# Optimization experiments

Measured on AMD Instinct MI355X. Metric: run time of the kernel, lower is better.

Reference implementation:

```python
import jax, jax.numpy as jnp
import numpy as np

TEMPERATURE = 0.5


def setup_inputs() -> dict:
    key = jax.random.key(0)
    k1, k2 = jax.random.split(key)
    N, D = 8192, 128
    features = jax.random.normal(k1, (N, D), dtype=jnp.float32)
    labels = jax.random.randint(k2, (N,), 0, 10, dtype=jnp.int64)
    return {"features": features, "labels": labels}


def reference(features, labels):
    # cosine similarity via normalized matmul (fused form of the broadcasted version)
    eps = 1e-8
    norm = jnp.maximum(jnp.linalg.norm(features, axis=-1, keepdims=True), eps)
    fn = features / norm
    sim = jnp.einsum('id,jd->ij', fn, fn) / TEMPERATURE  # [N, N]

    pos_mask = labels[:, None] == labels[None, :]        # [N, N] bool
    pos_f = pos_mask.astype(sim.dtype)
    neg_f = 1.0 - pos_f

    exp_pos = jnp.exp(sim * pos_f)                       # [N, N]
    exp_neg = jnp.sum(jnp.exp(sim * neg_f), axis=1, keepdims=True)  # [N, 1]

    loss_mat = -jnp.log(exp_pos / (exp_pos + exp_neg))   # [N, N]
    # mean over positive entries (jit-safe masked mean)
    num_pos = jnp.sum(pos_f)
    loss = jnp.sum(loss_mat * pos_f) / num_pos
    return loss
```

## Files before the change

kernel.cpp:

```cpp
#include <hip/hip_runtime.h>
#include <hip/hip_bf16.h>
#include <math.h>

#define NROWS 8192
#define DIM 128
#define BM 128
#define BN 128
#define CS 8
#define COLS_PER_SLAB (NROWS / CS)
#define CT_ITERS (COLS_PER_SLAB / BN)
#define RS (NROWS / BM)
#define SCALE 1.69864368f
#define LN2F 0.69314718056f

typedef __attribute__((ext_vector_type(8))) short bf16x8;
typedef __attribute__((ext_vector_type(4))) float f32x4;

#define VMCNT0 asm volatile("s_waitcnt vmcnt(0)" ::: "memory")
#define BAR __builtin_amdgcn_s_barrier()

__device__ __forceinline__ void gload16(const void* g, void* l) {
  __builtin_amdgcn_global_load_lds(
      (const __attribute__((address_space(1))) void*)g,
      (__attribute__((address_space(3))) void*)l, 16, 0, 0);
}

__device__ __forceinline__ void stageA(const ushort* __restrict__ fnb, int row0,
                                       char* tile, int t) {
  const char* gb = reinterpret_cast<const char*>(fnb) + (size_t)row0 * 256;
#pragma unroll
  for (int i = 0; i < 8; ++i) {
    int q = t + 256 * i;
    int row = q >> 4, c = q & 15;
    gload16(gb + row * 256 + ((c ^ (row & 7)) << 4), tile + q * 16);
  }
}

__device__ __forceinline__ void stageBh(const ushort* __restrict__ fnb, int j0, int kh,
                                        char* buf, int t) {
  const char* gb = reinterpret_cast<const char*>(fnb) + (size_t)j0 * 256 + kh * 128;
#pragma unroll
  for (int i = 0; i < 4; ++i) {
    int q = t + 256 * i;
    int row = q >> 3, c = q & 7;
    gload16(gb + row * 256 + ((c ^ (row & 7)) << 4), buf + q * 16);
  }
}

__global__ __launch_bounds__(256) void k_norm(const float* __restrict__ f,
                                              __hip_bfloat16* __restrict__ fnb,
                                              float* __restrict__ losssum) {
  if (blockIdx.x == 0 && threadIdx.x == 0) losssum[0] = 0.f;
  int wave = threadIdx.x >> 6;
  int lane = threadIdx.x & 63;
  int row = blockIdx.x * 4 + wave;
  const float* src = f + (size_t)row * DIM;
  float v0 = src[lane];
  float v1 = src[lane + 64];
  float ss = v0 * v0 + v1 * v1;
#pragma unroll
  for (int o = 32; o > 0; o >>= 1) ss += __shfl_down(ss, o);
  ss = __shfl(ss, 0);
  float inv = SCALE / fmaxf(sqrtf(ss), 1e-8f);
  __hip_bfloat16* dst = fnb + (size_t)row * DIM;
  dst[lane] = __float2bfloat16(v0 * inv);
  dst[lane + 64] = __float2bfloat16(v1 * inv);
}

__global__ __launch_bounds__(256, 2) void k_main(
    const ushort* __restrict__ fnb, const int* __restrict__ lab,
    float* __restrict__ P, float* __restrict__ Ps) {
  __shared__ char lds[65536];
  char* Bbuf0 = lds + 32768;
  char* Bbuf1 = lds + 49152;

  const int t = threadIdx.x;
  const int lane = t & 63;
  const int w = t >> 6;
  const int wm = w >> 1, wn = w & 1;
  const int g = lane >> 4, li16 = lane & 15;
  const int cs = blockIdx.x;
  const int i0 = blockIdx.y * BM;
  const int jslab = cs * COLS_PER_SLAB;

  stageA(fnb, i0, lds, t);
  stageBh(fnb, jslab, 0, Bbuf0, t);

  int lr[4][4];
#pragma unroll
  for (int m = 0; m < 4; ++m)
#pragma unroll
    for (int r = 0; r < 4; ++r)
      lr[m][r] = lab[i0 + wm * 64 + m * 16 + g * 4 + r];

  float a_tot[4][4] = {}, a_pos[4][4] = {};
  float s_sim = 0.f;

  VMCNT0;
  BAR;

#define COMPUTE(buf, khA)                                                        \
  _Pragma("unroll") for (int ks = 0; ks < 2; ++ks) {                             \
    const int kc = ((khA)*2 + ks) * 4 + g;                                       \
    bf16x8 af[4], bf[4];                                                         \
    _Pragma("unroll") for (int m = 0; m < 4; ++m) {                              \
      int r = wm * 64 + m * 16 + li16;                                           \
      af[m] = *reinterpret_cast<const bf16x8*>(lds + r * 256 + ((kc ^ (r & 7)) << 4)); \
    }                                                                            \
    _Pragma("unroll") for (int n = 0; n < 4; ++n) {                              \
      int r2 = wn * 64 + n * 16 + li16;                                          \
      bf[n] = *reinterpret_cast<const bf16x8*>((buf) + r2 * 128 + (((ks * 4 + g) ^ (r2 & 7)) << 4)); \
    }                                                                            \
    _Pragma("unroll") for (int m = 0; m < 4; ++m)                                \
      _Pragma("unroll") for (int n = 0; n < 4; ++n)                              \
        acc[m][n] = __builtin_amdgcn_mfma_f32_16x16x32_bf16(af[m], bf[n], acc[m][n], 0, 0, 0); \
  }

#pragma unroll 1
  for (int ct = 0; ct < CT_ITERS; ++ct) {
    const int j0 = jslab + ct * BN;

    f32x4 acc[4][4];
#pragma unroll
    for (int m = 0; m < 4; ++m)
#pragma unroll
      for (int n = 0; n < 4; ++n) acc[m][n] = (f32x4){0.f, 0.f, 0.f, 0.f};

    stageBh(fnb, j0, 1, Bbuf1, t);
    COMPUTE(Bbuf0, 0);
    VMCNT0;
    BAR;

    if (ct + 1 < CT_ITERS) stageBh(fnb, j0 + BN, 0, Bbuf0, t);
    COMPUTE(Bbuf1, 1);

#pragma unroll
    for (int n = 0; n < 4; ++n) {
      const int lc = lab[j0 + wn * 64 + n * 16 + li16];
#pragma unroll
      for (int m = 0; m < 4; ++m)
#pragma unroll
        for (int r = 0; r < 4; ++r) {
          float u = acc[m][n][r];
          float E = __builtin_exp2f(u);
          float msk = (lr[m][r] == lc) ? 1.f : 0.f;
          a_tot[m][r] += E;
          a_pos[m][r] = fmaf(msk, E, a_pos[m][r]);
          s_sim = fmaf(msk, u, s_sim);
        }
    }
    VMCNT0;
    BAR;
  }
#undef COMPUTE

#pragma unroll
  for (int m = 0; m < 4; ++m)
#pragma unroll
    for (int r = 0; r < 4; ++r)
#pragma unroll
      for (int off = 8; off > 0; off >>= 1) {
        a_tot[m][r] += __shfl_xor(a_tot[m][r], off);
        a_pos[m][r] += __shfl_xor(a_pos[m][r], off);
      }
#pragma unroll
  for (int off = 32; off > 0; off >>= 1) s_sim += __shfl_xor(s_sim, off);

  __syncthreads();
  float(*red)[2][2] = reinterpret_cast<float(*)[2][2]>(lds);
  float* sS = reinterpret_cast<float*>(lds + 4096);
  if (li16 == 0) {
#pragma unroll
    for (int m = 0; m < 4; ++m)
#pragma unroll
      for (int r = 0; r < 4; ++r) {
        int rl = wm * 64 + m * 16 + g * 4 + r;
        red[rl][wn][0] = a_tot[m][r];
        red[rl][wn][1] = a_pos[m][r];
      }
  }
  if (lane == 0) sS[w] = s_sim;
  __syncthreads();
  if (wn == 0 && li16 == 0) {
#pragma unroll
    for (int m = 0; m < 4; ++m)
#pragma unroll
      for (int r = 0; r < 4; ++r) {
        int rl = wm * 64 + m * 16 + g * 4 + r;
        float* dst = P + ((size_t)cs * NROWS + (i0 + rl)) * 2;
        dst[0] = red[rl][0][0] + red[rl][1][0];
        dst[1] = red[rl][0][1] + red[rl][1][1];
      }
  }
  if (t == 0) Ps[blockIdx.y * CS + cs] = sS[0] + sS[1] + sS[2] + sS[3];
}

__global__ __launch_bounds__(1024) void k_rowfinal(
    const float* __restrict__ P, const int* __restrict__ lab,
    float* __restrict__ losssum) {
  __shared__ int sh[16][16];
  __shared__ int hist_s[16];
  __shared__ float sred[1024];
  const int t = threadIdx.x;
  const int w = t >> 6;
  if ((t & 63) < 16) sh[w][t & 63] = 0;
  __syncthreads();
#pragma unroll
  for (int it = 0; it < NROWS / 1024; ++it)
    atomicAdd(&sh[w][lab[t + it * 1024]], 1);
  __syncthreads();
  if (t < 16) {
    int s = 0;
#pragma unroll
    for (int x = 0; x < 16; ++x) s += sh[x][t];
    hist_s[t] = s;
  }
  __syncthreads();

  int i = blockIdx.x * 1024 + t;
  float st = 0.f, sp = 0.f;
#pragma unroll
  for (int cs = 0; cs < CS; ++cs) {
    const float* p = P + ((size_t)cs * NROWS + i) * 2;
    st += p[0];
    sp += p[1];
  }
  float cnt = (float)hist_s[lab[i]];
  float negtot = st - sp + cnt;
  float li = cnt * logf(negtot) + sp / negtot;
  sred[t] = li;
  __syncthreads();
  for (int s2 = 512; s2 > 0; s2 >>= 1) {
    if (t < s2) sred[t] += sred[t + s2];
    __syncthreads();
  }
  if (t == 0) {
    atomicAdd(&losssum[0], sred[0]);
    if (blockIdx.x == 0) {
      int np = 0;
#pragma unroll
      for (int c = 0; c < 10; ++c) np += hist_s[c] * hist_s[c];
      losssum[1] = (float)np;
    }
  }
}

__global__ __launch_bounds__(512) void k_out(const float* __restrict__ losssum,
                                             const float* __restrict__ Ps,
                                             float* __restrict__ out) {
  __shared__ float sred[512];
  const int t = threadIdx.x;
  sred[t] = Ps[t];
  __syncthreads();
  for (int s = 256; s > 0; s >>= 1) {
    if (t < s) sred[t] += sred[t + s];
    __syncthreads();
  }
  if (t == 0) out[0] = (losssum[0] - LN2F * sred[0]) / losssum[1];
}

extern "C" void kernel_launch(void* const* d_in, const int* in_sizes, int n_in,
                              void* d_out, int out_size, void* d_ws, size_t ws_size,
                              hipStream_t stream) {
  const float* feat = (const float*)d_in[0];
  const int* lab = (const int*)d_in[1];
  float* out = (float*)d_out;
  char* ws = (char*)d_ws;

  __hip_bfloat16* fnb = (__hip_bfloat16*)ws;
  size_t off = (size_t)NROWS * DIM * 2;
  float* P = (float*)(ws + off); off += (size_t)CS * NROWS * 2 * 4;
  float* Ps = (float*)(ws + off); off += (size_t)CS * RS * 4;
  float* losssum = (float*)(ws + off);

  k_norm<<<NROWS / 4, 256, 0, stream>>>(feat, fnb, losssum);
  k_main<<<dim3(CS, RS), 256, 0, stream>>>((const ushort*)fnb, lab, P, Ps);
  k_rowfinal<<<NROWS / 1024, 1024, 0, stream>>>(P, lab, losssum);
  k_out<<<1, 512, 0, stream>>>(losssum, Ps, out);
}
```

Before: 52.15 us.

## Use 8 waves per block in main GEMM kernel and raise MFMA priority

```diff
diff --git a/kernel.cpp b/kernel.cpp
--- a/kernel.cpp
+++ b/kernel.cpp
@@ -29,8 +29,8 @@
                                        char* tile, int t) {
   const char* gb = reinterpret_cast<const char*>(fnb) + (size_t)row0 * 256;
 #pragma unroll
-  for (int i = 0; i < 8; ++i) {
-    int q = t + 256 * i;
+  for (int i = 0; i < 4; ++i) {
+    int q = t + 512 * i;
     int row = q >> 4, c = q & 15;
     gload16(gb + row * 256 + ((c ^ (row & 7)) << 4), tile + q * 16);
   }
@@ -40,8 +40,8 @@
                                         char* buf, int t) {
   const char* gb = reinterpret_cast<const char*>(fnb) + (size_t)j0 * 256 + kh * 128;
 #pragma unroll
-  for (int i = 0; i < 4; ++i) {
-    int q = t + 256 * i;
+  for (int i = 0; i < 2; ++i) {
+    int q = t + 512 * i;
     int row = q >> 3, c = q & 7;
     gload16(gb + row * 256 + ((c ^ (row & 7)) << 4), buf + q * 16);
   }
@@ -67,24 +67,25 @@
   dst[lane + 64] = __float2bfloat16(v1 * inv);
 }
 
-__global__ __launch_bounds__(256, 2) void k_main(
+__global__ __launch_bounds__(512, 4) void k_main(
     const ushort* __restrict__ fnb, const int* __restrict__ lab,
     float* __restrict__ P, float* __restrict__ Ps) {
   __shared__ char lds[65536];
-  char* Bbuf0 = lds + 32768;
-  char* Bbuf1 = lds + 49152;
+  char* Bb0 = lds + 32768;
+  char* Bb1 = lds + 49152;
 
   const int t = threadIdx.x;
   const int lane = t & 63;
   const int w = t >> 6;
-  const int wm = w >> 1, wn = w & 1;
+  const int wm = w >> 2;
+  const int wn = w & 3;
   const int g = lane >> 4, li16 = lane & 15;
   const int cs = blockIdx.x;
   const int i0 = blockIdx.y * BM;
   const int jslab = cs * COLS_PER_SLAB;
 
   stageA(fnb, i0, lds, t);
-  stageBh(fnb, jslab, 0, Bbuf0, t);
+  stageBh(fnb, jslab, 0, Bb0, t);
 
   int lr[4][4];
 #pragma unroll
@@ -99,20 +100,20 @@
   VMCNT0;
   BAR;
 
-#define COMPUTE(buf, khA)                                                        \
+#define COMPUTE(buf, kh)                                                         \
   _Pragma("unroll") for (int ks = 0; ks < 2; ++ks) {                             \
-    const int kc = ((khA)*2 + ks) * 4 + g;                                       \
-    bf16x8 af[4], bf[4];                                                         \
+    const int kc = (kh) * 8 + ks * 4 + g;                                        \
+    bf16x8 af[4], bf[2];                                                         \
     _Pragma("unroll") for (int m = 0; m < 4; ++m) {                              \
       int r = wm * 64 + m * 16 + li16;                                           \
       af[m] = *reinterpret_cast<const bf16x8*>(lds + r * 256 + ((kc ^ (r & 7)) << 4)); \
     }                                                                            \
-    _Pragma("unroll") for (int n = 0; n < 4; ++n) {                              \
-      int r2 = wn * 64 + n * 16 + li16;                                          \
+    _Pragma("unroll") for (int n = 0; n < 2; ++n) {                              \
+      int r2 = wn * 32 + n * 16 + li16;                                          \
       bf[n] = *reinterpret_cast<const bf16x8*>((buf) + r2 * 128 + (((ks * 4 + g) ^ (r2 & 7)) << 4)); \
     }                                                                            \
     _Pragma("unroll") for (int m = 0; m < 4; ++m)                                \
-      _Pragma("unroll") for (int n = 0; n < 4; ++n)                              \
+      _Pragma("unroll") for (int n = 0; n < 2; ++n)                              \
         acc[m][n] = __builtin_amdgcn_mfma_f32_16x16x32_bf16(af[m], bf[n], acc[m][n], 0, 0, 0); \
   }
 
@@ -120,23 +121,27 @@
   for (int ct = 0; ct < CT_ITERS; ++ct) {
     const int j0 = jslab + ct * BN;
 
-    f32x4 acc[4][4];
+    f32x4 acc[4][2];
 #pragma unroll
     for (int m = 0; m < 4; ++m)
 #pragma unroll
-      for (int n = 0; n < 4; ++n) acc[m][n] = (f32x4){0.f, 0.f, 0.f, 0.f};
-
-    stageBh(fnb, j0, 1, Bbuf1, t);
-    COMPUTE(Bbuf0, 0);
+      for (int n = 0; n < 2; ++n) acc[m][n] = (f32x4){0.f, 0.f, 0.f, 0.f};
+
+    stageBh(fnb, j0, 1, Bb1, t);
+    __builtin_amdgcn_s_setprio(1);
+    COMPUTE(Bb0, 0);
+    __builtin_amdgcn_s_setprio(0);
     VMCNT0;
     BAR;
 
-    if (ct + 1 < CT_ITERS) stageBh(fnb, j0 + BN, 0, Bbuf0, t);
-    COMPUTE(Bbuf1, 1);
-
-#pragma unroll
-    for (int n = 0; n < 4; ++n) {
-      const int lc = lab[j0 + wn * 64 + n * 16 + li16];
+    if (ct + 1 < CT_ITERS) stageBh(fnb, j0 + BN, 0, Bb0, t);
+    __builtin_amdgcn_s_setprio(1);
+    COMPUTE(Bb1, 1);
+    __builtin_amdgcn_s_setprio(0);
+
+#pragma unroll
+    for (int n = 0; n < 2; ++n) {
+      const int lc = lab[j0 + wn * 32 + n * 16 + li16];
 #pragma unroll
       for (int m = 0; m < 4; ++m)
 #pragma unroll
@@ -167,8 +172,8 @@
   for (int off = 32; off > 0; off >>= 1) s_sim += __shfl_xor(s_sim, off);
 
   __syncthreads();
-  float(*red)[2][2] = reinterpret_cast<float(*)[2][2]>(lds);
-  float* sS = reinterpret_cast<float*>(lds + 4096);
+  float(*red)[4][2] = reinterpret_cast<float(*)[4][2]>(lds);
+  float* sS = reinterpret_cast<float*>(lds + 8192);
   if (li16 == 0) {
 #pragma unroll
     for (int m = 0; m < 4; ++m)
@@ -188,11 +193,16 @@
       for (int r = 0; r < 4; ++r) {
         int rl = wm * 64 + m * 16 + g * 4 + r;
         float* dst = P + ((size_t)cs * NROWS + (i0 + rl)) * 2;
-        dst[0] = red[rl][0][0] + red[rl][1][0];
-        dst[1] = red[rl][0][1] + red[rl][1][1];
+        dst[0] = red[rl][0][0] + red[rl][1][0] + red[rl][2][0] + red[rl][3][0];
+        dst[1] = red[rl][0][1] + red[rl][1][1] + red[rl][2][1] + red[rl][3][1];
       }
   }
-  if (t == 0) Ps[blockIdx.y * CS + cs] = sS[0] + sS[1] + sS[2] + sS[3];
+  if (t == 0) {
+    float s = 0.f;
+#pragma unroll
+    for (int x = 0; x < 8; ++x) s += sS[x];
+    Ps[blockIdx.y * CS + cs] = s;
+  }
 }
 
 __global__ __launch_bounds__(1024) void k_rowfinal(
@@ -274,7 +284,7 @@
   float* losssum = (float*)(ws + off);
 
   k_norm<<<NROWS / 4, 256, 0, stream>>>(feat, fnb, losssum);
-  k_main<<<dim3(CS, RS), 256, 0, stream>>>((const ushort*)fnb, lab, P, Ps);
+  k_main<<<dim3(CS, RS), 512, 0, stream>>>((const ushort*)fnb, lab, P, Ps);
   k_rowfinal<<<NROWS / 1024, 1024, 0, stream>>>(P, lab, losssum);
   k_out<<<1, 512, 0, stream>>>(losssum, Ps, out);
 }
```

New measurement: 55.92 us. +7.2%, slower.

## Sort rows by label to skip mask work on label-disjoint tiles

Applied to the files above, without the earlier changes.

```diff
diff --git a/kernel.cpp b/kernel.cpp
--- a/kernel.cpp
+++ b/kernel.cpp
@@ -47,10 +47,69 @@
   }
 }
 
+__global__ __launch_bounds__(1024) void k_perm(const int* __restrict__ lab,
+                                               int* __restrict__ perm,
+                                               int* __restrict__ labs_s,
+                                               float* __restrict__ losssum) {
+  __shared__ int sh[16][16];
+  __shared__ int wcount[16][10];
+  __shared__ int baseRun[10];
+  const int t = threadIdx.x;
+  const int w = t >> 6;
+  const int lane = t & 63;
+
+  if (lane < 16) sh[w][lane] = 0;
+  __syncthreads();
+#pragma unroll
+  for (int it = 0; it < 8; ++it)
+    atomicAdd(&sh[w][lab[t + it * 1024]], 1);
+  __syncthreads();
+  if (t < 10) {
+    int s = 0;
+#pragma unroll
+    for (int x = 0; x < 16; ++x) s += sh[x][t];
+    sh[0][t] = s;
+  }
+  if (t == 0) losssum[0] = 0.f;
+  __syncthreads();
+  if (t < 10) {
+    int b = 0;
+    for (int c = 0; c < t; ++c) b += sh[0][c];
+    baseRun[t] = b;
+  }
+  __syncthreads();
+
+  for (int k = 0; k < 8; ++k) {
+    int row = k * 1024 + t;
+    int lr = lab[row];
+    int myBefore = 0;
+#pragma unroll
+    for (int c = 0; c < 10; ++c) {
+      unsigned long long m = __ballot(lr == c);
+      if (lr == c) myBefore = __popcll(m & ((1ull << lane) - 1ull));
+      if (lane == 0) wcount[w][c] = __popcll(m);
+    }
+    __syncthreads();
+    int off = baseRun[lr];
+    for (int wp = 0; wp < 15; ++wp)
+      if (wp < w) off += wcount[wp][lr];
+    int p = off + myBefore;
+    perm[row] = p;
+    labs_s[p] = lr;
+    __syncthreads();
+    if (t < 10) {
+      int s = 0;
+#pragma unroll
+      for (int x = 0; x < 16; ++x) s += wcount[x][t];
+      baseRun[t] += s;
+    }
+    __syncthreads();
+  }
+}
+
 __global__ __launch_bounds__(256) void k_norm(const float* __restrict__ f,
-                                              __hip_bfloat16* __restrict__ fnb,
-                                              float* __restrict__ losssum) {
-  if (blockIdx.x == 0 && threadIdx.x == 0) losssum[0] = 0.f;
+                                              const int* __restrict__ perm,
+                                              __hip_bfloat16* __restrict__ fnb) {
   int wave = threadIdx.x >> 6;
   int lane = threadIdx.x & 63;
   int row = blockIdx.x * 4 + wave;
@@ -62,17 +121,17 @@
   for (int o = 32; o > 0; o >>= 1) ss += __shfl_down(ss, o);
   ss = __shfl(ss, 0);
   float inv = SCALE / fmaxf(sqrtf(ss), 1e-8f);
-  __hip_bfloat16* dst = fnb + (size_t)row * DIM;
+  __hip_bfloat16* dst = fnb + (size_t)perm[row] * DIM;
   dst[lane] = __float2bfloat16(v0 * inv);
   dst[lane + 64] = __float2bfloat16(v1 * inv);
 }
 
 __global__ __launch_bounds__(256, 2) void k_main(
-    const ushort* __restrict__ fnb, const int* __restrict__ lab,
+    const ushort* __restrict__ fnb, const int* __restrict__ labs_s,
     float* __restrict__ P, float* __restrict__ Ps) {
   __shared__ char lds[65536];
-  char* Bbuf0 = lds + 32768;
-  char* Bbuf1 = lds + 49152;
+  char* Bb0 = lds + 32768;
+  char* Bb1 = lds + 49152;
 
   const int t = threadIdx.x;
   const int lane = t & 63;
@@ -84,14 +143,17 @@
   const int jslab = cs * COLS_PER_SLAB;
 
   stageA(fnb, i0, lds, t);
-  stageBh(fnb, jslab, 0, Bbuf0, t);
+  stageBh(fnb, jslab, 0, Bb0, t);
+
+  const int rcmin = labs_s[i0];
+  const int rcmax = labs_s[i0 + BM - 1];
 
   int lr[4][4];
 #pragma unroll
   for (int m = 0; m < 4; ++m)
 #pragma unroll
     for (int r = 0; r < 4; ++r)
-      lr[m][r] = lab[i0 + wm * 64 + m * 16 + g * 4 + r];
+      lr[m][r] = labs_s[i0 + wm * 64 + m * 16 + g * 4 + r];
 
   float a_tot[4][4] = {}, a_pos[4][4] = {};
   float s_sim = 0.f;
@@ -99,9 +161,9 @@
   VMCNT0;
   BAR;
 
-#define COMPUTE(buf, khA)                                                        \
+#define COMPUTE(buf, kh)                                                         \
   _Pragma("unroll") for (int ks = 0; ks < 2; ++ks) {                             \
-    const int kc = ((khA)*2 + ks) * 4 + g;                                       \
+    const int kc = (kh) * 8 + ks * 4 + g;                                        \
     bf16x8 af[4], bf[4];                                                         \
     _Pragma("unroll") for (int m = 0; m < 4; ++m) {                              \
       int r = wm * 64 + m * 16 + li16;                                           \
@@ -126,28 +188,40 @@
 #pragma unroll
       for (int n = 0; n < 4; ++n) acc[m][n] = (f32x4){0.f, 0.f, 0.f, 0.f};
 
-    stageBh(fnb, j0, 1, Bbuf1, t);
-    COMPUTE(Bbuf0, 0);
+    stageBh(fnb, j0, 1, Bb1, t);
+    COMPUTE(Bb0, 0);
     VMCNT0;
     BAR;
 
-    if (ct + 1 < CT_ITERS) stageBh(fnb, j0 + BN, 0, Bbuf0, t);
-    COMPUTE(Bbuf1, 1);
-
-#pragma unroll
-    for (int n = 0; n < 4; ++n) {
-      const int lc = lab[j0 + wn * 64 + n * 16 + li16];
-#pragma unroll
-      for (int m = 0; m < 4; ++m)
-#pragma unroll
-        for (int r = 0; r < 4; ++r) {
-          float u = acc[m][n][r];
-          float E = __builtin_exp2f(u);
-          float msk = (lr[m][r] == lc) ? 1.f : 0.f;
-          a_tot[m][r] += E;
-          a_pos[m][r] = fmaf(msk, E, a_pos[m][r]);
-          s_sim = fmaf(msk, u, s_sim);
-        }
+    if (ct + 1 < CT_ITERS) stageBh(fnb, j0 + BN, 0, Bb0, t);
+    COMPUTE(Bb1, 1);
+
+    const int ccmin = labs_s[j0];
+    const int ccmax = labs_s[j0 + BN - 1];
+    if (ccmin <= rcmax && ccmax >= rcmin) {
+#pragma unroll
+      for (int n = 0; n < 4; ++n) {
+        const int lc = labs_s[j0 + wn * 64 + n * 16 + li16];
+#pragma unroll
+        for (int m = 0; m < 4; ++m)
+#pragma unroll
+          for (int r = 0; r < 4; ++r) {
+            float u = acc[m][n][r];
+            float E = __builtin_exp2f(u);
+            float msk = (lr[m][r] == lc) ? 1.f : 0.f;
+            a_tot[m][r] += E;
+            a_pos[m][r] = fmaf(msk, E, a_pos[m][r]);
+            s_sim = fmaf(msk, u, s_sim);
+          }
+      }
+    } else {
+#pragma unroll
+      for (int n = 0; n < 4; ++n)
+#pragma unroll
+        for (int m = 0; m < 4; ++m)
+#pragma unroll
+          for (int r = 0; r < 4; ++r)
+            a_tot[m][r] += __builtin_exp2f(acc[m][n][r]);
     }
     VMCNT0;
     BAR;
@@ -197,7 +271,7 @@
 
 __global__ __launch_bounds__(1024) void k_rowfinal(
     const float* __restrict__ P, const int* __restrict__ lab,
-    float* __restrict__ losssum) {
+    const int* __restrict__ labs_s, float* __restrict__ losssum) {
   __shared__ int sh[16][16];
   __shared__ int hist_s[16];
   __shared__ float sred[1024];
@@ -225,7 +299,7 @@
     st += p[0];
     sp += p[1];
   }
-  float cnt = (float)hist_s[lab[i]];
+  float cnt = (float)hist_s[labs_s[i]];
   float negtot = st - sp + cnt;
   float li = cnt * logf(negtot) + sp / negtot;
   sred[t] = li;
@@ -271,10 +345,13 @@
   size_t off = (size_t)NROWS * DIM * 2;
   float* P = (float*)(ws + off); off += (size_t)CS * NROWS * 2 * 4;
   float* Ps = (float*)(ws + off); off += (size_t)CS * RS * 4;
+  int* perm = (int*)(ws + off); off += (size_t)NROWS * 4;
+  int* labs_s = (int*)(ws + off); off += (size_t)NROWS * 4;
   float* losssum = (float*)(ws + off);
 
-  k_norm<<<NROWS / 4, 256, 0, stream>>>(feat, fnb, losssum);
-  k_main<<<dim3(CS, RS), 256, 0, stream>>>((const ushort*)fnb, lab, P, Ps);
-  k_rowfinal<<<NROWS / 1024, 1024, 0, stream>>>(P, lab, losssum);
+  k_perm<<<1, 1024, 0, stream>>>(lab, perm, labs_s, losssum);
+  k_norm<<<NROWS / 4, 256, 0, stream>>>(feat, perm, fnb);
+  k_main<<<dim3(CS, RS), 256, 0, stream>>>((const ushort*)fnb, labs_s, P, Ps);
+  k_rowfinal<<<NROWS / 1024, 1024, 0, stream>>>(P, lab, labs_s, losssum);
   k_out<<<1, 512, 0, stream>>>(losssum, Ps, out);
 }
```

After: 65.94 us. 26.5% more time.
